# Performance work log

Hardware: AMD Instinct MI355X
Metric: run time of the kernel (lower is better)

The kernel has to match this reference:

```python
import jax, jax.numpy as jnp
import numpy as np

N = 8192
IN_DIM = 256
OUT_DIM = 256


def setup_inputs() -> dict:
    key = jax.random.key(0)
    k1, k2, k3, k4 = jax.random.split(key, 4)
    x = jax.random.normal(k1, (N, IN_DIM), dtype=jnp.float32)
    adj = jax.random.uniform(k2, (N, N), dtype=jnp.float32)
    # nn.Linear(in_dim, out_dim): weight [out,in], bias [out]. Store W as [in,out].
    bound = 1.0 / np.sqrt(IN_DIM)
    W = jax.random.uniform(k3, (IN_DIM, OUT_DIM), dtype=jnp.float32, minval=-bound, maxval=bound)
    b = jax.random.uniform(k4, (OUT_DIM,), dtype=jnp.float32, minval=-bound, maxval=bound)
    return {"x": x, "adj": adj, "W": W, "b": b}


def reference(x, adj, W, b):
    # ReLU( D^{-1/2} (A + I) D^{-1/2} X W + b )
    # A_hat = adj + I; degree = A_hat.sum(axis=1)
    n = adj.shape[0]
    A_hat = adj + jnp.eye(n, dtype=adj.dtype)
    degree = A_hat.sum(axis=1)
    d_inv_sqrt = degree ** -0.5  # [N]
    # D^{-1/2} @ A_hat @ D^{-1/2} == row-scale then col-scale (no NxN diag matmuls)
    A_norm = A_hat * d_inv_sqrt[:, None] * d_inv_sqrt[None, :]
    out = A_norm @ x          # [N, in_dim]
    out = out @ W + b         # [N, out_dim]
    return jax.nn.relu(out)
```

## Files before the change

kernel.cpp:

```cpp
#include <hip/hip_runtime.h>
#include <hip/hip_bf16.h>


typedef __attribute__((ext_vector_type(8))) short short8;
typedef __attribute__((ext_vector_type(4))) short short4v;
typedef __attribute__((ext_vector_type(4))) float floatx4;

#define GLDS16(g, l) __builtin_amdgcn_global_load_lds(\
    (const __attribute__((address_space(1))) void*)(g), \
    (__attribute__((address_space(3))) void*)(l), 16, 0, 0)

__device__ __forceinline__ unsigned short f2b(float f) {
  unsigned int x = __builtin_bit_cast(unsigned int, f);
  unsigned int r = (x + 0x7fffu + ((x >> 16) & 1u)) >> 16;
  return (unsigned short)r;
}

__global__ __launch_bounds__(256) void k_prep(
    const float* __restrict__ adj, const float* __restrict__ W,
    const float* __restrict__ X, float* __restrict__ s,
    unsigned short* __restrict__ WT, unsigned short* __restrict__ Xb) {
  __shared__ float part[4];
  const int b = blockIdx.x, t = threadIdx.x;
  if (b < 8192) {
    const float4* row = (const float4*)(adj + (size_t)b * 8192);
    float sum = 0.f;
#pragma unroll
    for (int q = 0; q < 8; ++q) {
      float4 v = row[t + q * 256];
      sum += v.x + v.y + v.z + v.w;
    }
#pragma unroll
    for (int o = 32; o > 0; o >>= 1) sum += __shfl_down(sum, o, 64);
    if ((t & 63) == 0) part[t >> 6] = sum;
    __syncthreads();
    if (t == 0) s[b] = rsqrtf(part[0] + part[1] + part[2] + part[3] + 1.0f);
  } else if (b < 8256) {
    const int wb = b - 8192;
#pragma unroll
    for (int q = 0; q < 4; ++q) {
      int i = wb * 1024 + q * 256 + t;
      WT[i] = f2b(W[(i & 255) * 256 + (i >> 8)]);
    }
  } else {
    const int xb = b - 8256;
#pragma unroll
    for (int q = 0; q < 8; ++q) {
      int i = xb * 2048 + q * 256 + t;
      Xb[i] = f2b(X[i]);
    }
  }
}

__global__ __launch_bounds__(256) void k_xw(
    const unsigned short* __restrict__ Xb, const unsigned short* __restrict__ WT,
    const float* __restrict__ bias, const float* __restrict__ s,
    float* __restrict__ Zd, unsigned short* __restrict__ ZsT) {
  __shared__ __align__(16) unsigned short ldsX[64 * 256];
  __shared__ __align__(16) unsigned short ldsW[64 * 256];
  const int t = threadIdx.x, l = t & 63, w = t >> 6;
  const int quad = l >> 4, nl = l & 15;
  const int m0 = blockIdx.x * 64, n0 = blockIdx.y * 64;
#pragma unroll
  for (int r = 0; r < 8; ++r) {
    int sl = r * 256 + t;
    int kc = sl >> 6, mm = sl & 63;
    GLDS16(Xb + (m0 + mm) * 256 + kc * 8, (char*)ldsX + sl * 16);
    GLDS16(WT + (n0 + mm) * 256 + kc * 8, (char*)ldsW + sl * 16);
  }
  __syncthreads();
  const int wm = w & 1, wn = w >> 1;
  floatx4 acc[2][2] = {};
#pragma unroll
  for (int kk = 0; kk < 8; ++kk) {
    int kc = kk * 4 + quad;
    short8 af[2], bf[2];
#pragma unroll
    for (int i = 0; i < 2; ++i) {
      af[i] = *(const short8*)&ldsX[(kc * 64 + wm * 32 + i * 16 + nl) * 8];
      bf[i] = *(const short8*)&ldsW[(kc * 64 + wn * 32 + i * 16 + nl) * 8];
    }
#pragma unroll
    for (int mi = 0; mi < 2; ++mi)
#pragma unroll
      for (int ni = 0; ni < 2; ++ni)
        acc[mi][ni] = __builtin_amdgcn_mfma_f32_16x16x32_bf16(af[mi], bf[ni], acc[mi][ni], 0, 0, 0);
  }
#pragma unroll
  for (int mi = 0; mi < 2; ++mi)
#pragma unroll
    for (int ni = 0; ni < 2; ++ni)
#pragma unroll
      for (int r = 0; r < 4; ++r) {
        int row = m0 + wm * 32 + mi * 16 + quad * 4 + r;
        int col = n0 + wn * 32 + ni * 16 + nl;
        float v = acc[mi][ni][r];
        float sr = s[row];
        Zd[row * 256 + col] = sr * sr * v + bias[col];
        ZsT[col * 8192 + row] = f2b(sr * v);
      }
}

__global__ __launch_bounds__(512) void k_main(
    const float* __restrict__ adj, const unsigned short* __restrict__ ZsT,
    const float* __restrict__ s, const float* __restrict__ Zd,
    float* __restrict__ out) {
  __shared__ __align__(16) char ldsA[8 * 544];
  __shared__ __align__(16) unsigned short ldsB[64 * 256];
  const int t = threadIdx.x, l = t & 63, w = t >> 6;
  const int quad = l >> 4, nl = l & 15;
  const int m0 = blockIdx.x * 32;
  const int aM = t >> 4, aC = t & 15;
  const float* aSrc = adj + (size_t)(m0 + aM) * 8192 + aC * 4;
  char* aDst = ldsA + (aC >> 1) * 544 + aM * 16 + (aC & 1) * 8;
  floatx4 acc[2][2] = {};
  for (int kt = 0; kt < 128; ++kt) {
    const int k0 = kt * 64;
    __syncthreads();
#pragma unroll
    for (int r = 0; r < 4; ++r) {
      int sl = r * 512 + t;
      GLDS16(ZsT + (sl & 255) * 8192 + k0 + (sl >> 8) * 8, (char*)ldsB + sl * 16);
    }
    float4 av = *(const float4*)(aSrc + k0);
    short4v ab = { (short)f2b(av.x), (short)f2b(av.y), (short)f2b(av.z), (short)f2b(av.w) };
    *(short4v*)aDst = ab;
    __syncthreads();
#pragma unroll
    for (int kk = 0; kk < 2; ++kk) {
      int kc = kk * 4 + quad;
      short8 af[2], bf[2];
      af[0] = *(const short8*)(ldsA + kc * 544 + nl * 16);
      af[1] = *(const short8*)(ldsA + kc * 544 + (16 + nl) * 16);
      bf[0] = *(const short8*)&ldsB[(kc * 256 + w * 32 + nl) * 8];
      bf[1] = *(const short8*)&ldsB[(kc * 256 + w * 32 + 16 + nl) * 8];
      acc[0][0] = __builtin_amdgcn_mfma_f32_16x16x32_bf16(af[0], bf[0], acc[0][0], 0, 0, 0);
      acc[0][1] = __builtin_amdgcn_mfma_f32_16x16x32_bf16(af[0], bf[1], acc[0][1], 0, 0, 0);
      acc[1][0] = __builtin_amdgcn_mfma_f32_16x16x32_bf16(af[1], bf[0], acc[1][0], 0, 0, 0);
      acc[1][1] = __builtin_amdgcn_mfma_f32_16x16x32_bf16(af[1], bf[1], acc[1][1], 0, 0, 0);
    }
  }
#pragma unroll
  for (int mi = 0; mi < 2; ++mi)
#pragma unroll
    for (int ni = 0; ni < 2; ++ni)
#pragma unroll
      for (int r = 0; r < 4; ++r) {
        int row = m0 + mi * 16 + quad * 4 + r;
        int col = w * 32 + ni * 16 + nl;
        float v = s[row] * acc[mi][ni][r] + Zd[row * 256 + col];
        out[row * 256 + col] = v > 0.f ? v : 0.f;
      }
}

extern "C" void kernel_launch(void* const* d_in, const int* in_sizes, int n_in,
                              void* d_out, int out_size, void* d_ws, size_t ws_size,
                              hipStream_t stream) {
  const float* X    = (const float*)d_in[0];
  const float* adj  = (const float*)d_in[1];
  const float* W    = (const float*)d_in[2];
  const float* bias = (const float*)d_in[3];
  float* out = (float*)d_out;

  char* ws = (char*)d_ws;
  float* s            = (float*)(ws);
  unsigned short* WT  = (unsigned short*)(ws + 32768);
  unsigned short* Xb  = (unsigned short*)(ws + 262144);
  float* Zd           = (float*)(ws + (8 << 20));
  unsigned short* ZsT = (unsigned short*)(ws + (16 << 20));

  hipLaunchKernelGGL(k_prep, dim3(9280), dim3(256), 0, stream, adj, W, X, s, WT, Xb);
  hipLaunchKernelGGL(k_xw, dim3(128, 4), dim3(256), 0, stream, Xb, WT, bias, s, Zd, ZsT);
  hipLaunchKernelGGL(k_main, dim3(256), dim3(512), 0, stream, adj, ZsT, s, Zd, out);
}
```

Before: 621.5 us.

## Pre-tile adj to bf16, split-K double-buffered main GEMM, scalar XW, finalize kernel

The prep kernel now reads adj once, computes degree partial sums with atomics, and writes a bf16 copy of adj in an MFMA-friendly tiled layout. The main kernel streams that pre-tiled bf16 adj and a tiled Z through double-buffered direct-to-LDS loads, with split-K over two halves and 64x128 output tiles. This gives 512 blocks instead of 256 and removes the fp32 adj read and in-loop conversion from the GEMM. A separate finalize kernel sums the two partials, scales, adds Zd and applies ReLU, and X@W is now done in fp32 scalar FMAs. The cost is an extra 128MB bf16 adj write plus reread, and extra partial-buffer traffic.

```diff
diff --git a/kernel.cpp b/kernel.cpp
--- a/kernel.cpp
+++ b/kernel.cpp
@@ -3,7 +3,6 @@
 
 
 typedef __attribute__((ext_vector_type(8))) short short8;
-typedef __attribute__((ext_vector_type(4))) short short4v;
 typedef __attribute__((ext_vector_type(4))) float floatx4;
 
 #define GLDS16(g, l) __builtin_amdgcn_global_load_lds(\
@@ -17,140 +16,171 @@
 }
 
 __global__ __launch_bounds__(256) void k_prep(
-    const float* __restrict__ adj, const float* __restrict__ W,
-    const float* __restrict__ X, float* __restrict__ s,
-    unsigned short* __restrict__ WT, unsigned short* __restrict__ Xb) {
-  __shared__ float part[4];
-  const int b = blockIdx.x, t = threadIdx.x;
-  if (b < 8192) {
-    const float4* row = (const float4*)(adj + (size_t)b * 8192);
-    float sum = 0.f;
-#pragma unroll
-    for (int q = 0; q < 8; ++q) {
-      float4 v = row[t + q * 256];
-      sum += v.x + v.y + v.z + v.w;
+    const float* __restrict__ adj, float* __restrict__ degree,
+    unsigned short* __restrict__ adjb) {
+  __shared__ float red[256];
+  const int t = threadIdx.x;
+  const int bg = blockIdx.x >> 2, kq = blockIdx.x & 3;
+  const int m0 = bg * 32;
+  const int row = m0 + (t & 31);
+  const int kc = t >> 5;
+  const float* src = adj + (size_t)row * 8192 + kq * 2048 + kc * 8;
+  unsigned short* dst = adjb +
+      ((((size_t)(row >> 6)) * 128 + kq * 32) * 512 + kc * 64 + (row & 63)) * 8;
+  float rs = 0.f;
+#pragma unroll 4
+  for (int kt = 0; kt < 32; ++kt) {
+    float4 a = *(const float4*)(src + kt * 64);
+    float4 b = *(const float4*)(src + kt * 64 + 4);
+    rs += a.x + a.y + a.z + a.w + b.x + b.y + b.z + b.w;
+    short8 u;
+    u[0] = (short)f2b(a.x); u[1] = (short)f2b(a.y);
+    u[2] = (short)f2b(a.z); u[3] = (short)f2b(a.w);
+    u[4] = (short)f2b(b.x); u[5] = (short)f2b(b.y);
+    u[6] = (short)f2b(b.z); u[7] = (short)f2b(b.w);
+    *(short8*)(dst + (size_t)kt * 512 * 8) = u;
+  }
+  red[t] = rs;
+  __syncthreads();
+  if (t < 32) {
+    float sum = red[t] + red[t + 32] + red[t + 64] + red[t + 96] +
+                red[t + 128] + red[t + 160] + red[t + 192] + red[t + 224];
+    atomicAdd(degree + m0 + t, sum);
+  }
+}
+
+__global__ __launch_bounds__(256) void k_xw(
+    const float* __restrict__ X, const float* __restrict__ W,
+    const float* __restrict__ bias, const float* __restrict__ degree,
+    float* __restrict__ Zd, unsigned short* __restrict__ Zsb) {
+  __shared__ unsigned short ldsT[256 * 36];
+  const int t = threadIdx.x, l = t & 63, w = t >> 6;
+  const int m0 = blockIdx.x * 32;
+  const int r0 = w * 8;
+  const int n0 = l * 4;
+  const float* Xp = X + (size_t)(m0 + r0) * 256;
+  float acc[8][4] = {};
+#pragma unroll 2
+  for (int k = 0; k < 256; k += 4) {
+    float4 wv[4];
+#pragma unroll
+    for (int j = 0; j < 4; ++j) wv[j] = *(const float4*)(W + (size_t)(k + j) * 256 + n0);
+#pragma unroll
+    for (int r = 0; r < 8; ++r) {
+      float4 xv = *(const float4*)(Xp + r * 256 + k);
+      const float xs[4] = {xv.x, xv.y, xv.z, xv.w};
+#pragma unroll
+      for (int j = 0; j < 4; ++j) {
+        acc[r][0] += xs[j] * wv[j].x;
+        acc[r][1] += xs[j] * wv[j].y;
+        acc[r][2] += xs[j] * wv[j].z;
+        acc[r][3] += xs[j] * wv[j].w;
+      }
     }
-#pragma unroll
-    for (int o = 32; o > 0; o >>= 1) sum += __shfl_down(sum, o, 64);
-    if ((t & 63) == 0) part[t >> 6] = sum;
-    __syncthreads();
-    if (t == 0) s[b] = rsqrtf(part[0] + part[1] + part[2] + part[3] + 1.0f);
-  } else if (b < 8256) {
-    const int wb = b - 8192;
-#pragma unroll
-    for (int q = 0; q < 4; ++q) {
-      int i = wb * 1024 + q * 256 + t;
-      WT[i] = f2b(W[(i & 255) * 256 + (i >> 8)]);
-    }
-  } else {
-    const int xb = b - 8256;
-#pragma unroll
-    for (int q = 0; q < 8; ++q) {
-      int i = xb * 2048 + q * 256 + t;
-      Xb[i] = f2b(X[i]);
-    }
-  }
-}
-
-__global__ __launch_bounds__(256) void k_xw(
-    const unsigned short* __restrict__ Xb, const unsigned short* __restrict__ WT,
-    const float* __restrict__ bias, const float* __restrict__ s,
-    float* __restrict__ Zd, unsigned short* __restrict__ ZsT) {
-  __shared__ __align__(16) unsigned short ldsX[64 * 256];
-  __shared__ __align__(16) unsigned short ldsW[64 * 256];
+  }
+  const float4 bv = *(const float4*)(bias + n0);
+  const int kt = m0 >> 6, hh = (m0 >> 5) & 1;
+#pragma unroll
+  for (int r = 0; r < 8; ++r) {
+    const int row = m0 + r0 + r;
+    const float sr = rsqrtf(degree[row] + 1.0f);
+    float4 zd;
+    zd.x = sr * sr * acc[r][0] + bv.x;
+    zd.y = sr * sr * acc[r][1] + bv.y;
+    zd.z = sr * sr * acc[r][2] + bv.z;
+    zd.w = sr * sr * acc[r][3] + bv.w;
+    *(float4*)(Zd + (size_t)row * 256 + n0) = zd;
+#pragma unroll
+    for (int n = 0; n < 4; ++n)
+      ldsT[(size_t)(n0 + n) * 36 + (r0 + r)] = f2b(sr * acc[r][n]);
+  }
+  __syncthreads();
+#pragma unroll
+  for (int c = 0; c < 4; ++c) {
+    const unsigned short* p = ldsT + (size_t)t * 36 + c * 8;
+    short8 vv;
+#pragma unroll
+    for (int j = 0; j < 8; ++j) vv[j] = p[j];
+    *(short8*)(Zsb + ((size_t)kt * 2048 + (hh * 4 + c) * 256 + t) * 8) = vv;
+  }
+}
+
+__global__ __launch_bounds__(512) void k_main(
+    const unsigned short* __restrict__ adjb, const unsigned short* __restrict__ Zsb,
+    float* __restrict__ P0, float* __restrict__ P1) {
+  __shared__ __align__(16) char lds[2][24576];
   const int t = threadIdx.x, l = t & 63, w = t >> 6;
   const int quad = l >> 4, nl = l & 15;
-  const int m0 = blockIdx.x * 64, n0 = blockIdx.y * 64;
-#pragma unroll
-  for (int r = 0; r < 8; ++r) {
-    int sl = r * 256 + t;
-    int kc = sl >> 6, mm = sl & 63;
-    GLDS16(Xb + (m0 + mm) * 256 + kc * 8, (char*)ldsX + sl * 16);
-    GLDS16(WT + (n0 + mm) * 256 + kc * 8, (char*)ldsW + sl * 16);
-  }
+  const int bm = blockIdx.x >> 2, sk = (blockIdx.x >> 1) & 1, nh = blockIdx.x & 1;
+  const int wm = w & 1, wn = w >> 1;
+  const unsigned short* aBase = adjb + ((size_t)bm * 128 + sk * 64) * 512 * 8;
+  const int sl0 = t, sl1 = 512 + t;
+  const size_t bU0 = (size_t)(sl0 >> 7) * 256 + nh * 128 + (sl0 & 127);
+  const size_t bU1 = (size_t)(sl1 >> 7) * 256 + nh * 128 + (sl1 & 127);
+  floatx4 acc[2][2] = {};
+
+  GLDS16(aBase + (size_t)t * 8, lds[0] + t * 16);
+  GLDS16(Zsb + ((size_t)(sk * 64) * 2048 + bU0) * 8, lds[0] + 8192 + sl0 * 16);
+  GLDS16(Zsb + ((size_t)(sk * 64) * 2048 + bU1) * 8, lds[0] + 8192 + sl1 * 16);
   __syncthreads();
-  const int wm = w & 1, wn = w >> 1;
-  floatx4 acc[2][2] = {};
-#pragma unroll
-  for (int kk = 0; kk < 8; ++kk) {
-    int kc = kk * 4 + quad;
-    short8 af[2], bf[2];
-#pragma unroll
-    for (int i = 0; i < 2; ++i) {
-      af[i] = *(const short8*)&ldsX[(kc * 64 + wm * 32 + i * 16 + nl) * 8];
-      bf[i] = *(const short8*)&ldsW[(kc * 64 + wn * 32 + i * 16 + nl) * 8];
-    }
-#pragma unroll
-    for (int mi = 0; mi < 2; ++mi)
-#pragma unroll
-      for (int ni = 0; ni < 2; ++ni)
-        acc[mi][ni] = __builtin_amdgcn_mfma_f32_16x16x32_bf16(af[mi], bf[ni], acc[mi][ni], 0, 0, 0);
-  }
-#pragma unroll
-  for (int mi = 0; mi < 2; ++mi)
-#pragma unroll
-    for (int ni = 0; ni < 2; ++ni)
-#pragma unroll
-      for (int r = 0; r < 4; ++r) {
-        int row = m0 + wm * 32 + mi * 16 + quad * 4 + r;
-        int col = n0 + wn * 32 + ni * 16 + nl;
-        float v = acc[mi][ni][r];
-        float sr = s[row];
-        Zd[row * 256 + col] = sr * sr * v + bias[col];
-        ZsT[col * 8192 + row] = f2b(sr * v);
-      }
-}
-
-__global__ __launch_bounds__(512) void k_main(
-    const float* __restrict__ adj, const unsigned short* __restrict__ ZsT,
-    const float* __restrict__ s, const float* __restrict__ Zd,
-    float* __restrict__ out) {
-  __shared__ __align__(16) char ldsA[8 * 544];
-  __shared__ __align__(16) unsigned short ldsB[64 * 256];
-  const int t = threadIdx.x, l = t & 63, w = t >> 6;
-  const int quad = l >> 4, nl = l & 15;
-  const int m0 = blockIdx.x * 32;
-  const int aM = t >> 4, aC = t & 15;
-  const float* aSrc = adj + (size_t)(m0 + aM) * 8192 + aC * 4;
-  char* aDst = ldsA + (aC >> 1) * 544 + aM * 16 + (aC & 1) * 8;
-  floatx4 acc[2][2] = {};
-  for (int kt = 0; kt < 128; ++kt) {
-    const int k0 = kt * 64;
-    __syncthreads();
-#pragma unroll
-    for (int r = 0; r < 4; ++r) {
-      int sl = r * 512 + t;
-      GLDS16(ZsT + (sl & 255) * 8192 + k0 + (sl >> 8) * 8, (char*)ldsB + sl * 16);
-    }
-    float4 av = *(const float4*)(aSrc + k0);
-    short4v ab = { (short)f2b(av.x), (short)f2b(av.y), (short)f2b(av.z), (short)f2b(av.w) };
-    *(short4v*)aDst = ab;
-    __syncthreads();
+
+  for (int kt = 0; kt < 64; ++kt) {
+    const int cur = kt & 1, nxt = cur ^ 1;
+    const int ktn = kt < 63 ? kt + 1 : 63;
+    GLDS16(aBase + ((size_t)ktn * 512 + t) * 8, lds[nxt] + t * 16);
+    GLDS16(Zsb + ((size_t)(sk * 64 + ktn) * 2048 + bU0) * 8, lds[nxt] + 8192 + sl0 * 16);
+    GLDS16(Zsb + ((size_t)(sk * 64 + ktn) * 2048 + bU1) * 8, lds[nxt] + 8192 + sl1 * 16);
+    const char* rA = lds[cur];
+    const char* rB = lds[cur] + 8192;
 #pragma unroll
     for (int kk = 0; kk < 2; ++kk) {
-      int kc = kk * 4 + quad;
+      const int kc = kk * 4 + quad;
       short8 af[2], bf[2];
-      af[0] = *(const short8*)(ldsA + kc * 544 + nl * 16);
-      af[1] = *(const short8*)(ldsA + kc * 544 + (16 + nl) * 16);
-      bf[0] = *(const short8*)&ldsB[(kc * 256 + w * 32 + nl) * 8];
-      bf[1] = *(const short8*)&ldsB[(kc * 256 + w * 32 + 16 + nl) * 8];
+      af[0] = *(const short8*)(rA + (kc * 64 + wm * 32 + nl) * 16);
+      af[1] = *(const short8*)(rA + (kc * 64 + wm * 32 + 16 + nl) * 16);
+      bf[0] = *(const short8*)(rB + (kc * 128 + wn * 32 + nl) * 16);
+      bf[1] = *(const short8*)(rB + (kc * 128 + wn * 32 + 16 + nl) * 16);
       acc[0][0] = __builtin_amdgcn_mfma_f32_16x16x32_bf16(af[0], bf[0], acc[0][0], 0, 0, 0);
       acc[0][1] = __builtin_amdgcn_mfma_f32_16x16x32_bf16(af[0], bf[1], acc[0][1], 0, 0, 0);
       acc[1][0] = __builtin_amdgcn_mfma_f32_16x16x32_bf16(af[1], bf[0], acc[1][0], 0, 0, 0);
       acc[1][1] = __builtin_amdgcn_mfma_f32_16x16x32_bf16(af[1], bf[1], acc[1][1], 0, 0, 0);
     }
-  }
+    __syncthreads();
+  }
+
+  float* P = sk ? P1 : P0;
 #pragma unroll
   for (int mi = 0; mi < 2; ++mi)
 #pragma unroll
     for (int ni = 0; ni < 2; ++ni)
 #pragma unroll
       for (int r = 0; r < 4; ++r) {
-        int row = m0 + mi * 16 + quad * 4 + r;
-        int col = w * 32 + ni * 16 + nl;
-        float v = s[row] * acc[mi][ni][r] + Zd[row * 256 + col];
-        out[row * 256 + col] = v > 0.f ? v : 0.f;
+        const int row = bm * 64 + wm * 32 + mi * 16 + quad * 4 + r;
+        const int col = nh * 128 + wn * 32 + ni * 16 + nl;
+        P[(size_t)row * 256 + col] = acc[mi][ni][r];
       }
+}
+
+__global__ __launch_bounds__(256) void k_fin(
+    const float* __restrict__ P0, const float* __restrict__ P1,
+    const float* __restrict__ Zd, const float* __restrict__ degree,
+    float* __restrict__ out) {
+  const int i = blockIdx.x * 256 + threadIdx.x;
+  const int row = i >> 6;
+  const float sr = rsqrtf(degree[row] + 1.0f);
+  const float4 p0 = *(const float4*)(P0 + (size_t)i * 4);
+  const float4 p1 = *(const float4*)(P1 + (size_t)i * 4);
+  const float4 zd = *(const float4*)(Zd + (size_t)i * 4);
+  float4 v;
+  v.x = sr * (p0.x + p1.x) + zd.x;
+  v.y = sr * (p0.y + p1.y) + zd.y;
+  v.z = sr * (p0.z + p1.z) + zd.z;
+  v.w = sr * (p0.w + p1.w) + zd.w;
+  v.x = v.x > 0.f ? v.x : 0.f;
+  v.y = v.y > 0.f ? v.y : 0.f;
+  v.z = v.z > 0.f ? v.z : 0.f;
+  v.w = v.w > 0.f ? v.w : 0.f;
+  *(float4*)(out + (size_t)i * 4) = v;
 }
 
 extern "C" void kernel_launch(void* const* d_in, const int* in_sizes, int n_in,
@@ -161,15 +191,18 @@
   const float* W    = (const float*)d_in[2];
   const float* bias = (const float*)d_in[3];
   float* out = (float*)d_out;
-
   char* ws = (char*)d_ws;
-  float* s            = (float*)(ws);
-  unsigned short* WT  = (unsigned short*)(ws + 32768);
-  unsigned short* Xb  = (unsigned short*)(ws + 262144);
-  float* Zd           = (float*)(ws + (8 << 20));
-  unsigned short* ZsT = (unsigned short*)(ws + (16 << 20));
-
-  hipLaunchKernelGGL(k_prep, dim3(9280), dim3(256), 0, stream, adj, W, X, s, WT, Xb);
-  hipLaunchKernelGGL(k_xw, dim3(128, 4), dim3(256), 0, stream, Xb, WT, bias, s, Zd, ZsT);
-  hipLaunchKernelGGL(k_main, dim3(256), dim3(512), 0, stream, adj, ZsT, s, Zd, out);
-}
+
+  float* degree        = (float*)(ws);
+  float* Zd            = (float*)(ws + (1 << 20));
+  unsigned short* Zsb  = (unsigned short*)(ws + (9 << 20));
+  float* P0            = (float*)(ws + (13 << 20));
+  float* P1            = (float*)(ws + (21 << 20));
+  unsigned short* adjb = (unsigned short*)(ws + ((size_t)29 << 20));
+
+  hipMemsetAsync(degree, 0, 8192 * sizeof(float), stream);
+  hipLaunchKernelGGL(k_prep, dim3(1024), dim3(256), 0, stream, adj, degree, adjb);
+  hipLaunchKernelGGL(k_xw, dim3(256), dim3(256), 0, stream, X, W, bias, degree, Zd, Zsb);
+  hipLaunchKernelGGL(k_main, dim3(512), dim3(512), 0, stream, adjb, Zsb, P0, P1);
+  hipLaunchKernelGGL(k_fin, dim3(2048), dim3(256), 0, stream, P0, P1, Zd, degree, out);
+}
```

After: 526.5 us. 15.3% less time.
